# Performance work log

Hardware: AMD Instinct MI355X
Metric: run time of the kernel (lower is better)

The kernel has to match this reference:

```python
import jax, jax.numpy as jnp
import numpy as np

N, DIM = 131072, 128
LEVELS, K = 3, 1024
BETA = 0.25
USAGE_REG = 1e-3


def setup_inputs() -> dict:
    key = jax.random.key(0)
    kx, kc = jax.random.split(key)
    x = jax.random.normal(kx, (N, DIM), dtype=jnp.float32)
    # nn.init.uniform_(emb.weight, -1/K, 1/K)
    codebooks = jax.random.uniform(kc, (LEVELS, K, DIM), dtype=jnp.float32,
                                   minval=-1.0 / K, maxval=1.0 / K)
    return {"x": x, "codebooks": codebooks}


def _quantize(x, W):
    d = (jnp.sum(x * x, axis=-1, keepdims=True)
         - 2.0 * jnp.matmul(x, W.T)
         + jnp.sum(W * W, axis=-1))
    idx = jnp.argmin(d, axis=-1)            # [N]
    q = W[idx]                              # gather -> [N, DIM]
    probs = jax.nn.softmax(-d, axis=-1)     # [N, K]
    return q, idx, probs


def reference(x, codebooks):
    sg = jax.lax.stop_gradient
    residual = x
    quantized_sum = jnp.zeros_like(x)
    codes = []
    commit_loss = jnp.zeros((), dtype=x.dtype)
    usage_loss = jnp.zeros((), dtype=x.dtype)
    for level in range(LEVELS):
        q, idx, probs = _quantize(residual, codebooks[level])
        quantized_sum = quantized_sum + q
        codes.append(idx)
        commit_loss = commit_loss + jnp.mean((sg(residual) - q) ** 2)
        commit_loss = commit_loss + BETA * jnp.mean((residual - sg(q)) ** 2)
        avg_probs = jnp.mean(probs, axis=0)  # [K]
        kl = jnp.sum(avg_probs * jnp.log(avg_probs * K + 1e-8))
        usage_loss = usage_loss + USAGE_REG * kl
        residual = residual - q
    codes = jnp.stack(codes, axis=-1)        # [N, LEVELS]
    # straight-through estimator
    quantized_final = quantized_sum + (residual - sg(residual))
    return quantized_final, codes, commit_loss, usage_loss
```

## Files before the change

kernel.cpp:

```cpp
#include <hip/hip_runtime.h>


#define NROWS   131072
#define DIMS    128
#define KCODES  1024
#define NLEV    3

#define QF_OFF   ((size_t)NROWS * DIMS)
#define CODE_OFF QF_OFF
#define SCAL_OFF (QF_OFF + (size_t)NROWS * 3)

#define WS_COMMIT_OFF 12288
#define WS_WK_OFF     12320
#define WS_WT_OFF     24608

__global__ __launch_bounds__(256) void init_acc(float* avgp, double* commit) {
    for (int i = threadIdx.x; i < 3072; i += 256) avgp[i] = 0.0f;
    if (threadIdx.x < 3) commit[threadIdx.x] = 0.0;
}

__global__ __launch_bounds__(256) void wnorm_kernel(const float* __restrict__ W,
                                                    float* __restrict__ wk) {
    const int wave = threadIdx.x >> 6, lane = threadIdx.x & 63;
    const int c = blockIdx.x * 4 + wave;
    const float2 v = *(const float2*)(W + (size_t)c * DIMS + 2 * lane);
    float s = v.x * v.x + v.y * v.y;
#pragma unroll
    for (int m = 32; m >= 1; m >>= 1) s += __shfl_xor(s, m, 64);
    if (lane == 0) wk[c] = s;
}

__global__ __launch_bounds__(256) void transpose_w(const float* __restrict__ W,
                                                   float* __restrict__ WT) {
    __shared__ float tile[32][65];
    const int l = blockIdx.z, k0 = blockIdx.y * 32, c0 = blockIdx.x * 64;
    const float* Wl = W + (size_t)l * KCODES * DIMS;
    float* WTl = WT + (size_t)l * DIMS * KCODES;
    {
        const int ci = threadIdx.x >> 2;
        const int kg = (threadIdx.x & 3) * 8;
        const float4 a = *(const float4*)(Wl + (size_t)(c0 + ci) * DIMS + k0 + kg);
        const float4 b = *(const float4*)(Wl + (size_t)(c0 + ci) * DIMS + k0 + kg + 4);
        tile[kg + 0][ci] = a.x; tile[kg + 1][ci] = a.y;
        tile[kg + 2][ci] = a.z; tile[kg + 3][ci] = a.w;
        tile[kg + 4][ci] = b.x; tile[kg + 5][ci] = b.y;
        tile[kg + 6][ci] = b.z; tile[kg + 7][ci] = b.w;
    }
    __syncthreads();
    {
        const int k = threadIdx.x >> 3;
        const int cg = (threadIdx.x & 7) * 8;
        float4 o0, o1;
        o0.x = tile[k][cg + 0]; o0.y = tile[k][cg + 1];
        o0.z = tile[k][cg + 2]; o0.w = tile[k][cg + 3];
        o1.x = tile[k][cg + 4]; o1.y = tile[k][cg + 5];
        o1.z = tile[k][cg + 6]; o1.w = tile[k][cg + 7];
        *(float4*)(WTl + (size_t)(k0 + k) * KCODES + c0 + cg)     = o0;
        *(float4*)(WTl + (size_t)(k0 + k) * KCODES + c0 + cg + 4) = o1;
    }
}

__global__ __launch_bounds__(512) void rvq_level(
    const float* __restrict__ x, const float* __restrict__ W,
    const float* __restrict__ WT, const float* __restrict__ wk,
    float* __restrict__ out, float* __restrict__ avgp,
    double* __restrict__ commit, const int level) {

    __shared__ float Wtile[2][4096];
    __shared__ float rowT[128][20];
    __shared__ float redf[16][17];
    __shared__ float Srow[16];
    __shared__ float wminv[16][8];
    __shared__ int   wmini[16][8];
    __shared__ float rowmin[16];
    __shared__ float wsum[16][8];
    __shared__ float rcpL[16];

    const int t = threadIdx.x;
    const int wave = t >> 6, lane = t & 63;
    const int c = wave * 128 + lane * 2;
    const size_t base = (size_t)blockIdx.x * 16;
    const float* codesF = out + CODE_OFF;
    const float* WTl = WT + (size_t)level * DIMS * KCODES;
    const float* wkl = wk + level * KCODES;

    if (t < 256) {
        const int r = t >> 4, i = t & 15;
        const size_t n = base + r;
        float4 v0 = *(const float4*)(x + n * DIMS + i * 8);
        float4 v1 = *(const float4*)(x + n * DIMS + i * 8 + 4);
        for (int j = 0; j < level; ++j) {
            const int idx = (int)codesF[n * 3 + j];
            const float* q = W + ((size_t)(j * KCODES + idx)) * DIMS + i * 8;
            const float4 q0 = *(const float4*)q;
            const float4 q1 = *(const float4*)(q + 4);
            v0.x = __fsub_rn(v0.x, q0.x); v0.y = __fsub_rn(v0.y, q0.y);
            v0.z = __fsub_rn(v0.z, q0.z); v0.w = __fsub_rn(v0.w, q0.w);
            v1.x = __fsub_rn(v1.x, q1.x); v1.y = __fsub_rn(v1.y, q1.y);
            v1.z = __fsub_rn(v1.z, q1.z); v1.w = __fsub_rn(v1.w, q1.w);
        }
        rowT[i * 8 + 0][r] = v0.x; rowT[i * 8 + 1][r] = v0.y;
        rowT[i * 8 + 2][r] = v0.z; rowT[i * 8 + 3][r] = v0.w;
        rowT[i * 8 + 4][r] = v1.x; rowT[i * 8 + 5][r] = v1.y;
        rowT[i * 8 + 6][r] = v1.z; rowT[i * 8 + 7][r] = v1.w;
        float sq = v0.x * v0.x + v0.y * v0.y + v0.z * v0.z + v0.w * v0.w
                 + v1.x * v1.x + v1.y * v1.y + v1.z * v1.z + v1.w * v1.w;
        redf[r][i] = sq;
    }
    __syncthreads();
    if (t < 16) {
        float s = 0.f;
        for (int i = 0; i < 16; ++i) s += redf[t][i];
        Srow[t] = s;
    }

    float2 acc[16];
#pragma unroll
    for (int r = 0; r < 16; ++r) { acc[r].x = 0.f; acc[r].y = 0.f; }

    {
        const float4 g0 = *(const float4*)(WTl + (size_t)t * 4);
        const float4 g1 = *(const float4*)(WTl + 2048 + (size_t)t * 4);
        *(float4*)&Wtile[0][t * 4]        = g0;
        *(float4*)&Wtile[0][2048 + t * 4] = g1;
    }
    __syncthreads();

    int buf = 0;
#pragma unroll 1
    for (int kt = 0; kt < 32; ++kt) {
        const float* Wn = WTl + (size_t)((kt + 1 < 32) ? (kt + 1) : 0) * 4096;
        const float4 g0 = *(const float4*)(Wn + (size_t)t * 4);
        const float4 g1 = *(const float4*)(Wn + 2048 + (size_t)t * 4);

        const float* Wt = &Wtile[buf][0];
#pragma unroll
        for (int kl = 0; kl < 4; ++kl) {
            const int k = kt * 4 + kl;
            const float2 wv = *(const float2*)&Wt[kl * 1024 + c];
#pragma unroll
            for (int rr = 0; rr < 4; ++rr) {
                const float4 rv = *(const float4*)&rowT[k][rr * 4];
                acc[rr * 4 + 0].x = fmaf(rv.x, wv.x, acc[rr * 4 + 0].x);
                acc[rr * 4 + 0].y = fmaf(rv.x, wv.y, acc[rr * 4 + 0].y);
                acc[rr * 4 + 1].x = fmaf(rv.y, wv.x, acc[rr * 4 + 1].x);
                acc[rr * 4 + 1].y = fmaf(rv.y, wv.y, acc[rr * 4 + 1].y);
                acc[rr * 4 + 2].x = fmaf(rv.z, wv.x, acc[rr * 4 + 2].x);
                acc[rr * 4 + 2].y = fmaf(rv.z, wv.y, acc[rr * 4 + 2].y);
                acc[rr * 4 + 3].x = fmaf(rv.w, wv.x, acc[rr * 4 + 3].x);
                acc[rr * 4 + 3].y = fmaf(rv.w, wv.y, acc[rr * 4 + 3].y);
            }
        }

        *(float4*)&Wtile[buf ^ 1][t * 4]        = g0;
        *(float4*)&Wtile[buf ^ 1][2048 + t * 4] = g1;
        __syncthreads();
        buf ^= 1;
    }

    const float2 wkv = *(const float2*)(wkl + c);
#pragma unroll
    for (int r = 0; r < 16; ++r) {
        const float Sr = Srow[r];
        float dx = __fadd_rn(__fsub_rn(Sr, __fmul_rn(2.0f, acc[r].x)), wkv.x);
        float dy = __fadd_rn(__fsub_rn(Sr, __fmul_rn(2.0f, acc[r].y)), wkv.y);
        acc[r].x = dx; acc[r].y = dy;
        float v = dx; int bi = c;
        if (dy < v) { v = dy; bi = c + 1; }
#pragma unroll
        for (int m = 1; m < 64; m <<= 1) {
            const float vo = __shfl_xor(v, m, 64);
            const int   io = __shfl_xor(bi, m, 64);
            if (vo < v || (vo == v && io < bi)) { v = vo; bi = io; }
        }
        if (lane == 0) { wminv[r][wave] = v; wmini[r][wave] = bi; }
    }
    __syncthreads();
    if (t < 16) {
        float v = wminv[t][0]; int bi = wmini[t][0];
        for (int w = 1; w < 8; ++w) {
            const float vo = wminv[t][w]; const int io = wmini[t][w];
            if (vo < v || (vo == v && io < bi)) { v = vo; bi = io; }
        }
        rowmin[t] = v;
        out[CODE_OFF + (base + t) * 3 + level] = (float)bi;
    }
    __syncthreads();

#pragma unroll
    for (int r = 0; r < 16; ++r) {
        const float mn = rowmin[r];
        const float ex = expf(__fsub_rn(mn, acc[r].x));
        const float ey = expf(__fsub_rn(mn, acc[r].y));
        acc[r].x = ex; acc[r].y = ey;
        float s = ex + ey;
#pragma unroll
        for (int m = 1; m < 64; m <<= 1) s += __shfl_xor(s, m, 64);
        if (lane == 0) wsum[r][wave] = s;
    }
    __syncthreads();
    if (t < 16) {
        float L = 0.f;
        for (int w = 0; w < 8; ++w) L += wsum[t][w];
        rcpL[t] = 1.0f / L;
    }
    if (t == 64) {
        double cs = 0.0;
        for (int r = 0; r < 16; ++r) cs += (double)rowmin[r];
        atomicAdd(&commit[level], cs);
    }
    __syncthreads();

    {
        float s0 = 0.f, s1 = 0.f;
#pragma unroll
        for (int r = 0; r < 16; ++r) {
            const float rl = rcpL[r];
            s0 = fmaf(acc[r].x, rl, s0);
            s1 = fmaf(acc[r].y, rl, s1);
        }
        atomicAdd(&avgp[level * KCODES + c + 0], s0);
        atomicAdd(&avgp[level * KCODES + c + 1], s1);
    }
}

__global__ __launch_bounds__(256) void finalize_kernel(const float* __restrict__ avgp,
                                                       const double* __restrict__ commit,
                                                       float* __restrict__ out) {
    __shared__ double red[256];
    __shared__ float  kls[3];
    const int t = threadIdx.x;
    for (int l = 0; l < 3; ++l) {
        double p = 0.0;
        for (int k = t; k < KCODES; k += 256) {
            const float avg = avgp[l * KCODES + k] * (1.0f / 131072.0f);
            p += (double)avg * log((double)avg * 1024.0 + 1e-8);
        }
        red[t] = p; __syncthreads();
        for (int off = 128; off >= 1; off >>= 1) {
            if (t < off) red[t] += red[t + off];
            __syncthreads();
        }
        if (t == 0) kls[l] = (float)red[0];
        __syncthreads();
    }
    if (t == 0) {
        float cv = 0.f, u = 0.f;
        for (int l = 0; l < 3; ++l) {
            const float m = (float)(commit[l] * (1.0 / 16777216.0));
            cv = __fadd_rn(cv, m);
            cv = __fadd_rn(cv, __fmul_rn(0.25f, m));
            u = __fadd_rn(u, __fmul_rn(1e-3f, kls[l]));
        }
        out[SCAL_OFF]     = cv;
        out[SCAL_OFF + 1] = u;
    }
}

__global__ __launch_bounds__(256) void gather_kernel(const float* __restrict__ W,
                                                     float* __restrict__ out) {
    const size_t g = (size_t)blockIdx.x * 256 + threadIdx.x;
    const size_t n = g >> 5;
    const int f = (int)(g & 31);
    const float* codes = out + CODE_OFF + n * 3;
    const int c0 = (int)codes[0], c1 = (int)codes[1], c2 = (int)codes[2];
    const float4 a = *(const float4*)(W + (size_t)c0 * DIMS + 4 * f);
    const float4 b = *(const float4*)(W + (size_t)(KCODES + c1) * DIMS + 4 * f);
    const float4 c = *(const float4*)(W + (size_t)(2 * KCODES + c2) * DIMS + 4 * f);
    float4 o;
    o.x = __fadd_rn(__fadd_rn(a.x, b.x), c.x);
    o.y = __fadd_rn(__fadd_rn(a.y, b.y), c.y);
    o.z = __fadd_rn(__fadd_rn(a.z, b.z), c.z);
    o.w = __fadd_rn(__fadd_rn(a.w, b.w), c.w);
    *(float4*)(out + n * DIMS + 4 * f) = o;
}

extern "C" void kernel_launch(void* const* d_in, const int* in_sizes, int n_in,
                              void* d_out, int out_size, void* d_ws, size_t ws_size,
                              hipStream_t stream) {
    const float* x = (const float*)d_in[0];
    const float* W = (const float*)d_in[1];
    float* out = (float*)d_out;
    float*  avgp   = (float*)d_ws;
    double* commit = (double*)((char*)d_ws + WS_COMMIT_OFF);
    float*  wkp    = (float*)((char*)d_ws + WS_WK_OFF);
    float*  WT     = (float*)((char*)d_ws + WS_WT_OFF);

    hipLaunchKernelGGL(init_acc, dim3(1), dim3(256), 0, stream, avgp, commit);
    hipLaunchKernelGGL(wnorm_kernel, dim3(768), dim3(256), 0, stream, W, wkp);
    hipLaunchKernelGGL(transpose_w, dim3(16, 4, 3), dim3(256), 0, stream, W, WT);
    for (int l = 0; l < NLEV; ++l)
        hipLaunchKernelGGL(rvq_level, dim3(NROWS / 16), dim3(512), 0, stream,
                           x, W, WT, wkp, out, avgp, commit, l);
    hipLaunchKernelGGL(finalize_kernel, dim3(1), dim3(256), 0, stream, avgp, commit, out);
    hipLaunchKernelGGL(gather_kernel, dim3((NROWS * 32) / 256), dim3(256), 0, stream, W, out);
}
```

Measured before the change: 2.402 ms.

## Halve W tile staging, split argmin reduction, use fast exp

The shared-memory W tile shrinks from 4096 to 2048 floats per buffer, which halves LDS use and doubles the number of k-loop iterations, with one sync per two k rows. The argmin butterfly is split into a float-min pass followed by an integer-min pass on the index, which cuts the shuffle-and-compare work per step. expf is replaced with the fast __expf intrinsic in the softmax step. The extra barriers may cost time, and __expf slightly changes precision of the usage probabilities.

```diff
diff --git a/kernel.cpp b/kernel.cpp
--- a/kernel.cpp
+++ b/kernel.cpp
@@ -66,7 +66,7 @@
     float* __restrict__ out, float* __restrict__ avgp,
     double* __restrict__ commit, const int level) {
 
-    __shared__ float Wtile[2][4096];
+    __shared__ float Wtile[2][2048];
     __shared__ float rowT[128][20];
     __shared__ float redf[16][17];
     __shared__ float Srow[16];
@@ -118,29 +118,21 @@
 #pragma unroll
     for (int r = 0; r < 16; ++r) { acc[r].x = 0.f; acc[r].y = 0.f; }
 
-    {
-        const float4 g0 = *(const float4*)(WTl + (size_t)t * 4);
-        const float4 g1 = *(const float4*)(WTl + 2048 + (size_t)t * 4);
-        *(float4*)&Wtile[0][t * 4]        = g0;
-        *(float4*)&Wtile[0][2048 + t * 4] = g1;
-    }
+    *(float4*)&Wtile[0][t * 4] = *(const float4*)(WTl + t * 4);
     __syncthreads();
 
     int buf = 0;
 #pragma unroll 1
-    for (int kt = 0; kt < 32; ++kt) {
-        const float* Wn = WTl + (size_t)((kt + 1 < 32) ? (kt + 1) : 0) * 4096;
-        const float4 g0 = *(const float4*)(Wn + (size_t)t * 4);
-        const float4 g1 = *(const float4*)(Wn + 2048 + (size_t)t * 4);
+    for (int kt = 0; kt < 64; ++kt) {
+        const float* Wn = WTl + (size_t)((kt + 1 < 64) ? (kt + 1) : 0) * 2048;
+        const float4 g = *(const float4*)(Wn + t * 4);
 
         const float* Wt = &Wtile[buf][0];
-#pragma unroll
-        for (int kl = 0; kl < 4; ++kl) {
-            const int k = kt * 4 + kl;
-            const float2 wv = *(const float2*)&Wt[kl * 1024 + c];
+        {
+            const float2 wv = *(const float2*)&Wt[c];
 #pragma unroll
             for (int rr = 0; rr < 4; ++rr) {
-                const float4 rv = *(const float4*)&rowT[k][rr * 4];
+                const float4 rv = *(const float4*)&rowT[2 * kt][rr * 4];
                 acc[rr * 4 + 0].x = fmaf(rv.x, wv.x, acc[rr * 4 + 0].x);
                 acc[rr * 4 + 0].y = fmaf(rv.x, wv.y, acc[rr * 4 + 0].y);
                 acc[rr * 4 + 1].x = fmaf(rv.y, wv.x, acc[rr * 4 + 1].x);
@@ -151,9 +143,23 @@
                 acc[rr * 4 + 3].y = fmaf(rv.w, wv.y, acc[rr * 4 + 3].y);
             }
         }
-
-        *(float4*)&Wtile[buf ^ 1][t * 4]        = g0;
-        *(float4*)&Wtile[buf ^ 1][2048 + t * 4] = g1;
+        {
+            const float2 wv = *(const float2*)&Wt[1024 + c];
+#pragma unroll
+            for (int rr = 0; rr < 4; ++rr) {
+                const float4 rv = *(const float4*)&rowT[2 * kt + 1][rr * 4];
+                acc[rr * 4 + 0].x = fmaf(rv.x, wv.x, acc[rr * 4 + 0].x);
+                acc[rr * 4 + 0].y = fmaf(rv.x, wv.y, acc[rr * 4 + 0].y);
+                acc[rr * 4 + 1].x = fmaf(rv.y, wv.x, acc[rr * 4 + 1].x);
+                acc[rr * 4 + 1].y = fmaf(rv.y, wv.y, acc[rr * 4 + 1].y);
+                acc[rr * 4 + 2].x = fmaf(rv.z, wv.x, acc[rr * 4 + 2].x);
+                acc[rr * 4 + 2].y = fmaf(rv.z, wv.y, acc[rr * 4 + 2].y);
+                acc[rr * 4 + 3].x = fmaf(rv.w, wv.x, acc[rr * 4 + 3].x);
+                acc[rr * 4 + 3].y = fmaf(rv.w, wv.y, acc[rr * 4 + 3].y);
+            }
+        }
+
+        *(float4*)&Wtile[buf ^ 1][t * 4] = g;
         __syncthreads();
         buf ^= 1;
     }
@@ -165,23 +171,23 @@
         float dx = __fadd_rn(__fsub_rn(Sr, __fmul_rn(2.0f, acc[r].x)), wkv.x);
         float dy = __fadd_rn(__fsub_rn(Sr, __fmul_rn(2.0f, acc[r].y)), wkv.y);
         acc[r].x = dx; acc[r].y = dy;
-        float v = dx; int bi = c;
-        if (dy < v) { v = dy; bi = c + 1; }
-#pragma unroll
-        for (int m = 1; m < 64; m <<= 1) {
-            const float vo = __shfl_xor(v, m, 64);
-            const int   io = __shfl_xor(bi, m, 64);
-            if (vo < v || (vo == v && io < bi)) { v = vo; bi = io; }
-        }
+        float v = fminf(dx, dy);
+#pragma unroll
+        for (int m = 1; m < 64; m <<= 1) v = fminf(v, __shfl_xor(v, m, 64));
+        int bi = 0x7FFFFFFF;
+        if (dy == v) bi = c + 1;
+        if (dx == v) bi = c;
+#pragma unroll
+        for (int m = 1; m < 64; m <<= 1) bi = min(bi, __shfl_xor(bi, m, 64));
         if (lane == 0) { wminv[r][wave] = v; wmini[r][wave] = bi; }
     }
     __syncthreads();
     if (t < 16) {
-        float v = wminv[t][0]; int bi = wmini[t][0];
-        for (int w = 1; w < 8; ++w) {
-            const float vo = wminv[t][w]; const int io = wmini[t][w];
-            if (vo < v || (vo == v && io < bi)) { v = vo; bi = io; }
-        }
+        float v = wminv[t][0];
+        for (int w = 1; w < 8; ++w) v = fminf(v, wminv[t][w]);
+        int bi = 0x7FFFFFFF;
+        for (int w = 7; w >= 0; --w)
+            if (wminv[t][w] == v) bi = (wmini[t][w] < bi) ? wmini[t][w] : bi;
         rowmin[t] = v;
         out[CODE_OFF + (base + t) * 3 + level] = (float)bi;
     }
@@ -190,8 +196,8 @@
 #pragma unroll
     for (int r = 0; r < 16; ++r) {
         const float mn = rowmin[r];
-        const float ex = expf(__fsub_rn(mn, acc[r].x));
-        const float ey = expf(__fsub_rn(mn, acc[r].y));
+        const float ex = __expf(__fsub_rn(mn, acc[r].x));
+        const float ey = __expf(__fsub_rn(mn, acc[r].y));
         acc[r].x = ex; acc[r].y = ey;
         float s = ex + ey;
 #pragma unroll
```

Result: faster. 2.209 ms (-8.1%).
